# Kernel tuning notes

Hardware: AMD Instinct MI355X
Metric: run time of the kernel (lower is better)

The kernel has to match this reference:

```python
import jax, jax.numpy as jnp
import numpy as np

PIXEL_THRESHOLD = 0.4
FRACTION_THRESHOLD = 0.03
NUM_CLASSES = 20
N, H, W = 100, 640, 960
LOGIT_SCALE = 8.0  # makes the instance-axis softmax peaky enough to cross PIXEL_THRESHOLD


def setup_inputs() -> dict:
    key = jax.random.key(0)
    k1, k2, k3 = jax.random.split(key, 3)
    cls_prob = jax.random.uniform(k1, (N,), dtype=jnp.float32)
    mask_prob = jax.random.normal(k2, (N, H, W), dtype=jnp.float32) * LOGIT_SCALE
    cls_idx = jax.random.randint(k3, (N,), 0, NUM_CLASSES)
    return {"cls_prob": cls_prob, "mask_prob": mask_prob, "cls_idx": cls_idx}


def _mask_removal(cls_prob, mask_prob, cls_idx):
    # Sort instances by class confidence, descending (greedy NMS order).
    order = jnp.argsort(-cls_prob)
    cls_prob_s = cls_prob[order]          # [N]
    cls_idx_s = cls_idx[order]            # [N]
    raw_s = mask_prob[order]              # [N,H,W] pre-softmax logits (mask_prob_copy)
    # Per-pixel softmax over the instance axis (permutation-equivariant, so
    # softmax-then-sort == sort-then-softmax as in the original).
    sm = jax.nn.softmax(raw_s, axis=0)    # [N,H,W]

    def step(state, inp):
        panoptic, mask_image = state      # [H,W], [C,H,W]
        smi, rawi, ci = inp
        logit = (smi >= PIXEL_THRESHOLD).astype(rawi.dtype)   # binarized mask [H,W]
        mask_sum = logit.sum()
        curr = mask_image[ci]
        overlap = jnp.sum((curr >= 1.0) & (logit == 1.0)).astype(rawi.dtype) / jnp.maximum(mask_sum, 1.0)
        degenerate = (logit.max() == logit.min()) | (mask_sum == 0.0)
        skip = degenerate | (overlap > FRACTION_THRESHOLD)
        # assign only unclaimed panoptic pixels inside the binarized mask
        assign = (panoptic == 0.0) & (logit == 1.0) & jnp.logical_not(skip)
        keep_mask = jnp.where(assign, rawi, 0.0)              # use_mask_low_constant=False
        panoptic = jnp.where(assign, 1.0, panoptic)
        mask_image = mask_image.at[ci].add(jnp.where(assign, logit, 0.0))
        return (panoptic, mask_image), (keep_mask, jnp.logical_not(skip))

    init = (jnp.zeros((H, W), jnp.float32), jnp.zeros((NUM_CLASSES, H, W), jnp.float32))
    _, (keep_masks, keep_flags) = jax.lax.scan(step, init, (sm, raw_s, cls_idx_s))
    # Fixed-shape outputs: keep_flags marks which (sorted) instances survived;
    # dropped instances have all-zero keep_masks rows.
    return cls_prob_s, keep_masks, cls_idx_s, keep_flags


def reference(cls_prob, mask_prob, cls_idx):
    return _mask_removal(cls_prob, mask_prob, cls_idx)
```

## Files before the change

kernel.cpp:

```cpp
#include <hip/hip_runtime.h>
#include <cstdint>
#include <cstddef>

#define N_INST 100
#define HW (640 * 960)
#define PIX_THR 0.4f
#define FRAC_THR 0.03f
#define EPS_BORDER 5e-5f
#define FLAG_CAP 65536
#define L2E 1.4426950408889634f

#define CB 1200
#define ZB 680
#define GRID (CB + ZB)
#define CHUNK_F4 15360
#define CHUNK_ITER 120
#define NCHUNK 1000
#define FIN_BLOCKS 128

#define OUT_MASKS_OFF 100
#define OUT_CLSIDX_OFF (100 + (size_t)N_INST * HW)
#define OUT_FLAGS_OFF (100 + (size_t)N_INST * HW + N_INST)


__global__ __launch_bounds__(256) void k0_init(
    const float* __restrict__ cls_prob,
    const int* __restrict__ cls_idx,
    int* __restrict__ ord,
    int* __restrict__ rank_arr,
    float* __restrict__ out,
    unsigned* __restrict__ mask_sum,
    unsigned* __restrict__ ctrs,
    unsigned* __restrict__ pair_cnt) {
    int t = threadIdx.x;
    if (t < N_INST) {
        float pi = cls_prob[t];
        int rank = 0;
        for (int j = 0; j < N_INST; ++j) {
            float pj = cls_prob[j];
            rank += (pj > pi) || (pj == pi && j < t);
        }
        ord[rank] = t;
        rank_arr[t] = rank;
        out[rank] = pi;
        out[OUT_CLSIDX_OFF + rank] = (float)cls_idx[t];
        mask_sum[t] = 0u;
    }
    if (t < 3) ctrs[t] = 0u;
    for (int i = t; i < N_INST * N_INST; i += 256)
        pair_cnt[i] = 0u;
}

__global__ __launch_bounds__(128) void k1_fused(
    const float* __restrict__ mask,
    const int* __restrict__ rank_arr,
    unsigned* __restrict__ mask_sum,
    unsigned* __restrict__ pair_cnt,
    uint4* __restrict__ pvals,
    unsigned* __restrict__ flag_count,
    unsigned* __restrict__ flag_list,
    unsigned* __restrict__ zctr,
    float* __restrict__ out) {
    int t = threadIdx.x;
    __shared__ unsigned s_chunk;

    if (blockIdx.x < CB) {
        __shared__ int srank[N_INST];
        __shared__ unsigned ssum[N_INST];
        if (t < N_INST) {
            srank[t] = rank_arr[t];
            ssum[t] = 0u;
        }
        __syncthreads();

        int p0 = (blockIdx.x * 128 + t) * 4;
        const float* base = mask + p0;

        float S[4] = {0.0f, 0.0f, 0.0f, 0.0f};
        float m[4] = {-3.4e38f, -3.4e38f, -3.4e38f, -3.4e38f};
        float n[4] = {-3.4e38f, -3.4e38f, -3.4e38f, -3.4e38f};
        int ia[4] = {0, 0, 0, 0};
        int ib[4] = {0, 0, 0, 0};

#pragma unroll 10
        for (int i = 0; i < N_INST; ++i) {
            float4 v4 = *(const float4*)(base + (size_t)i * HW);
            float vv[4] = {v4.x, v4.y, v4.z, v4.w};
#pragma unroll
            for (int j = 0; j < 4; ++j) {
                float v = vv[j];
                S[j] += exp2f(v * L2E);
                bool gt = v > m[j];
                bool g2 = v > n[j];
                n[j] = fmaxf(n[j], fminf(m[j], v));
                ib[j] = gt ? ia[j] : (g2 ? i : ib[j]);
                ia[j] = gt ? i : ia[j];
                m[j] = fmaxf(m[j], v);
            }
        }

#pragma unroll
        for (int j = 0; j < 4; ++j) {
            int p = p0 + j;
            float e1 = exp2f(m[j] * L2E);
            float e2 = exp2f(n[j] * L2E);
            float t04 = 0.4f * S[j];
            float w = EPS_BORDER * S[j];
            bool q1 = e1 >= t04;
            bool border = (fabsf(e1 - t04) < w) || (q1 && fabsf(e2 - t04) < w);

            unsigned c = 0u;
            float vlo = 0.0f, vhi = 0.0f;
            if (border) {
                unsigned slot = atomicAdd(flag_count, 1u);
                if (slot < FLAG_CAP) flag_list[slot] = (unsigned)p;
            } else if (q1) {
                bool q2 = e2 >= t04;
                int r1 = srank[ia[j]];
                atomicAdd(&ssum[r1], 1u);
                if (q2) {
                    int r2 = srank[ib[j]];
                    atomicAdd(&ssum[r2], 1u);
                    int lo = min(r1, r2), hi = max(r1, r2);
                    atomicAdd(&pair_cnt[lo * N_INST + hi], 1u);
                    c = (unsigned)(lo + 1) | ((unsigned)(hi + 1) << 8);
                    vlo = (r1 < r2) ? m[j] : n[j];
                    vhi = (r1 < r2) ? n[j] : m[j];
                } else {
                    c = (unsigned)(r1 + 1);
                    vlo = m[j];
                }
            }
            pvals[p] = make_uint4(c, __float_as_uint(vlo), __float_as_uint(vhi), 0u);
        }

        __syncthreads();
        if (t < N_INST && ssum[t] != 0u)
            atomicAdd(&mask_sum[t], ssum[t]);
    }

    for (;;) {
        if (t == 0) s_chunk = atomicAdd(zctr, 1u);
        __syncthreads();
        unsigned c = s_chunk;
        __syncthreads();
        if (c >= NCHUNK) break;
        float4* dst = (float4*)(out + OUT_MASKS_OFF) + (size_t)c * CHUNK_F4 + t;
        const float4 z4 = make_float4(0.0f, 0.0f, 0.0f, 0.0f);
#pragma unroll 8
        for (int k = 0; k < CHUNK_ITER; ++k)
            dst[k * 128] = z4;
    }
}

__global__ __launch_bounds__(256) void k2_finish(
    const float* __restrict__ mask,
    const int* __restrict__ ord,
    const int* __restrict__ cls_idx,
    unsigned* __restrict__ mask_sum,
    unsigned* __restrict__ pair_cnt,
    uint4* __restrict__ pvals,
    const unsigned* __restrict__ flag_count,
    const unsigned* __restrict__ flag_list,
    unsigned* __restrict__ done,
    int* __restrict__ keep,
    float* __restrict__ out) {
    __shared__ int sord[N_INST];
    __shared__ unsigned s_last;
    int t = threadIdx.x;
    if (t < N_INST) sord[t] = ord[t];
    __syncthreads();

    unsigned nf = *flag_count;
    if (nf > FLAG_CAP) nf = FLAG_CAP;
    for (unsigned idx = blockIdx.x * 256 + t; idx < nf;
         idx += FIN_BLOCKS * 256) {
        int p = (int)flag_list[idx];
        float v[N_INST];
#pragma unroll
        for (int i = 0; i < N_INST; ++i)
            v[i] = mask[(size_t)sord[i] * HW + p];

        float m = v[0];
        int p1 = 0;
        float m2 = -3.4e38f;
        int p2 = 0;
#pragma unroll
        for (int i = 1; i < N_INST; ++i) {
            if (v[i] > m) { m2 = m; p2 = p1; m = v[i]; p1 = i; }
            else if (v[i] > m2) { m2 = v[i]; p2 = i; }
        }
        float d = 0.0f;
#pragma unroll
        for (int i = 0; i < N_INST; ++i)
            d += expf(v[i] - m);

        float sm1 = 1.0f / d;
        float sm2 = expf(m2 - m) / d;
        bool q1 = (sm1 >= PIX_THR);
        bool q2 = (sm2 >= PIX_THR);
        unsigned c = 0u;
        float vlo = 0.0f, vhi = 0.0f;
        if (q1) {
            atomicAdd(&mask_sum[p1], 1u);
            if (q2) {
                atomicAdd(&mask_sum[p2], 1u);
                int lo = min(p1, p2), hi = max(p1, p2);
                atomicAdd(&pair_cnt[lo * N_INST + hi], 1u);
                c = (unsigned)(lo + 1) | ((unsigned)(hi + 1) << 8);
                vlo = v[lo];
                vhi = v[hi];
            } else {
                c = (unsigned)(p1 + 1);
                vlo = v[p1];
            }
        }
        pvals[p] = make_uint4(c, __float_as_uint(vlo), __float_as_uint(vhi), 0u);
    }

    __threadfence();
    if (t == 0) s_last = atomicAdd(done, 1u);
    __syncthreads();
    if (s_last != FIN_BLOCKS - 1) return;
    __threadfence();

    __shared__ unsigned spair[N_INST * N_INST];
    __shared__ int scls[N_INST];
    __shared__ unsigned sms[N_INST];
    __shared__ int skeep[N_INST];
    for (int i = t; i < N_INST * N_INST; i += 256)
        spair[i] = pair_cnt[i];
    if (t < N_INST) {
        scls[t] = cls_idx[sord[t]];
        sms[t] = mask_sum[t];
    }
    __syncthreads();

    for (int b = 0; b < N_INST; ++b) {
        if (t < 64) {
            unsigned cnt = 0u;
            for (int a = t; a < b; a += 64)
                if (skeep[a] && scls[a] == scls[b])
                    cnt += spair[a * N_INST + b];
#pragma unroll
            for (int off = 32; off; off >>= 1)
                cnt += __shfl_down((int)cnt, off);
            if (t == 0) {
                unsigned ms = sms[b];
                float overlap = (float)cnt / fmaxf((float)ms, 1.0f);
                bool degen = (ms == 0u) || (ms == (unsigned)HW);
                bool skip = degen || (overlap > FRAC_THR);
                skeep[b] = skip ? 0 : 1;
            }
        }
        __syncthreads();
    }

    if (t < N_INST) {
        keep[t] = skeep[t];
        out[OUT_FLAGS_OFF + t] = (float)skeep[t];
    }
}

__global__ __launch_bounds__(256) void k3_scatter(
    const uint4* __restrict__ pvals,
    const int* __restrict__ keep,
    float* __restrict__ out) {
    __shared__ int skeep[N_INST];
    if (threadIdx.x < N_INST) skeep[threadIdx.x] = keep[threadIdx.x];
    __syncthreads();

    int p = blockIdx.x * 256 + threadIdx.x;
    uint4 pv = pvals[p];
    unsigned c = pv.x;
    if (c == 0u) return;
    int a = (int)(c & 0xFFu) - 1;
    int b = (int)(c >> 8) - 1;

    int inst;
    float val;
    if (skeep[a]) {
        inst = a;
        val = __uint_as_float(pv.y);
    } else if (b >= 0 && skeep[b]) {
        inst = b;
        val = __uint_as_float(pv.z);
    } else {
        return;
    }
    out[OUT_MASKS_OFF + (size_t)inst * HW + p] = val;
}

extern "C" void kernel_launch(void* const* d_in, const int* in_sizes, int n_in,
                              void* d_out, int out_size, void* d_ws, size_t ws_size,
                              hipStream_t stream) {
    const float* cls_prob = (const float*)d_in[0];
    const float* mask = (const float*)d_in[1];
    const int* cls_idx = (const int*)d_in[2];
    float* out = (float*)d_out;

    char* ws = (char*)d_ws;
    int* ord = (int*)(ws + 0);
    int* rank_arr = (int*)(ws + 512);
    int* keep = (int*)(ws + 1024);
    unsigned* mask_sum = (unsigned*)(ws + 1536);
    unsigned* ctrs = (unsigned*)(ws + 2048);
    unsigned* pair_cnt = (unsigned*)(ws + 4096);
    uint4* pvals = (uint4*)(ws + 65536);
    unsigned* flag_list = (unsigned*)(ws + 65536 + (size_t)HW * 16);

    unsigned* flag_count = &ctrs[0];
    unsigned* zctr = &ctrs[1];
    unsigned* done = &ctrs[2];

    k0_init<<<1, 256, 0, stream>>>(cls_prob, cls_idx, ord, rank_arr, out,
                                   mask_sum, ctrs, pair_cnt);
    k1_fused<<<GRID, 128, 0, stream>>>(mask, rank_arr, mask_sum, pair_cnt,
                                       pvals, flag_count, flag_list, zctr, out);
    k2_finish<<<FIN_BLOCKS, 256, 0, stream>>>(mask, ord, cls_idx, mask_sum,
                                              pair_cnt, pvals, flag_count,
                                              flag_list, done, keep, out);
    k3_scatter<<<HW / 256, 256, 0, stream>>>(pvals, keep, out);
}
```

Baseline: 259.6 us.

## Fold border-pixel fixup and greedy keep decision into the main kernel's last block

Merges the separate finish kernel into the main fused kernel: the last block to finish, found with a done counter, re-evaluates flagged border pixels and runs the sequential greedy keep/skip scan. This removes one kernel launch and its gap. The number of zeroing blocks also drops. In exchange, the border fixup now runs on a single 128-thread block instead of 128 blocks. It re-reads the 100 logits per pixel twice rather than caching them in registers, and the pair counts are read from global memory instead of shared memory, which could lengthen the serial tail.

```diff
diff --git a/kernel.cpp b/kernel.cpp
--- a/kernel.cpp
+++ b/kernel.cpp
@@ -11,12 +11,11 @@
 #define L2E 1.4426950408889634f
 
 #define CB 1200
-#define ZB 680
+#define ZB 480
 #define GRID (CB + ZB)
 #define CHUNK_F4 15360
 #define CHUNK_ITER 120
 #define NCHUNK 1000
-#define FIN_BLOCKS 128
 
 #define OUT_MASKS_OFF 100
 #define OUT_CLSIDX_OFF (100 + (size_t)N_INST * HW)
@@ -51,25 +50,32 @@
         pair_cnt[i] = 0u;
 }
 
-__global__ __launch_bounds__(128) void k1_fused(
+__global__ __launch_bounds__(128) void k1_mega(
     const float* __restrict__ mask,
     const int* __restrict__ rank_arr,
+    const int* __restrict__ ord,
+    const int* __restrict__ cls_idx,
     unsigned* __restrict__ mask_sum,
     unsigned* __restrict__ pair_cnt,
     uint4* __restrict__ pvals,
     unsigned* __restrict__ flag_count,
     unsigned* __restrict__ flag_list,
     unsigned* __restrict__ zctr,
+    unsigned* __restrict__ done,
+    int* __restrict__ keep,
     float* __restrict__ out) {
     int t = threadIdx.x;
     __shared__ unsigned s_chunk;
+    __shared__ unsigned s_last;
+    __shared__ int s_i[N_INST];
+    __shared__ unsigned s_u[N_INST];
+    __shared__ int scls[N_INST];
+    __shared__ int skp[N_INST];
 
     if (blockIdx.x < CB) {
-        __shared__ int srank[N_INST];
-        __shared__ unsigned ssum[N_INST];
         if (t < N_INST) {
-            srank[t] = rank_arr[t];
-            ssum[t] = 0u;
+            s_i[t] = rank_arr[t];
+            s_u[t] = 0u;
         }
         __syncthreads();
 
@@ -116,11 +122,11 @@
                 if (slot < FLAG_CAP) flag_list[slot] = (unsigned)p;
             } else if (q1) {
                 bool q2 = e2 >= t04;
-                int r1 = srank[ia[j]];
-                atomicAdd(&ssum[r1], 1u);
+                int r1 = s_i[ia[j]];
+                atomicAdd(&s_u[r1], 1u);
                 if (q2) {
-                    int r2 = srank[ib[j]];
-                    atomicAdd(&ssum[r2], 1u);
+                    int r2 = s_i[ib[j]];
+                    atomicAdd(&s_u[r2], 1u);
                     int lo = min(r1, r2), hi = max(r1, r2);
                     atomicAdd(&pair_cnt[lo * N_INST + hi], 1u);
                     c = (unsigned)(lo + 1) | ((unsigned)(hi + 1) << 8);
@@ -135,8 +141,8 @@
         }
 
         __syncthreads();
-        if (t < N_INST && ssum[t] != 0u)
-            atomicAdd(&mask_sum[t], ssum[t]);
+        if (t < N_INST && s_u[t] != 0u)
+            atomicAdd(&mask_sum[t], s_u[t]);
     }
 
     for (;;) {
@@ -151,50 +157,31 @@
         for (int k = 0; k < CHUNK_ITER; ++k)
             dst[k * 128] = z4;
     }
-}
-
-__global__ __launch_bounds__(256) void k2_finish(
-    const float* __restrict__ mask,
-    const int* __restrict__ ord,
-    const int* __restrict__ cls_idx,
-    unsigned* __restrict__ mask_sum,
-    unsigned* __restrict__ pair_cnt,
-    uint4* __restrict__ pvals,
-    const unsigned* __restrict__ flag_count,
-    const unsigned* __restrict__ flag_list,
-    unsigned* __restrict__ done,
-    int* __restrict__ keep,
-    float* __restrict__ out) {
-    __shared__ int sord[N_INST];
-    __shared__ unsigned s_last;
-    int t = threadIdx.x;
-    if (t < N_INST) sord[t] = ord[t];
-    __syncthreads();
-
+
+    __threadfence();
+    if (t == 0) s_last = atomicAdd(done, 1u);
+    __syncthreads();
+    if (s_last != GRID - 1) return;
+    __threadfence();
+
+    if (t < N_INST) s_i[t] = ord[t];
+    __syncthreads();
     unsigned nf = *flag_count;
     if (nf > FLAG_CAP) nf = FLAG_CAP;
-    for (unsigned idx = blockIdx.x * 256 + t; idx < nf;
-         idx += FIN_BLOCKS * 256) {
+    for (unsigned idx = t; idx < nf; idx += 128) {
         int p = (int)flag_list[idx];
-        float v[N_INST];
-#pragma unroll
-        for (int i = 0; i < N_INST; ++i)
-            v[i] = mask[(size_t)sord[i] * HW + p];
-
-        float m = v[0];
-        int p1 = 0;
-        float m2 = -3.4e38f;
-        int p2 = 0;
-#pragma unroll
-        for (int i = 1; i < N_INST; ++i) {
-            if (v[i] > m) { m2 = m; p2 = p1; m = v[i]; p1 = i; }
-            else if (v[i] > m2) { m2 = v[i]; p2 = i; }
+        float m = -3.4e38f, m2 = -3.4e38f;
+        int p1 = 0, p2 = 0;
+        for (int i = 0; i < N_INST; ++i) {
+            float v = mask[(size_t)s_i[i] * HW + p];
+            if (v > m) { m2 = m; p2 = p1; m = v; p1 = i; }
+            else if (v > m2) { m2 = v; p2 = i; }
         }
         float d = 0.0f;
-#pragma unroll
-        for (int i = 0; i < N_INST; ++i)
-            d += expf(v[i] - m);
-
+        for (int i = 0; i < N_INST; ++i) {
+            float v = mask[(size_t)s_i[i] * HW + p];
+            d += expf(v - m);
+        }
         float sm1 = 1.0f / d;
         float sm2 = expf(m2 - m) / d;
         bool q1 = (sm1 >= PIX_THR);
@@ -208,31 +195,21 @@
                 int lo = min(p1, p2), hi = max(p1, p2);
                 atomicAdd(&pair_cnt[lo * N_INST + hi], 1u);
                 c = (unsigned)(lo + 1) | ((unsigned)(hi + 1) << 8);
-                vlo = v[lo];
-                vhi = v[hi];
+                vlo = (lo == p1) ? m : m2;
+                vhi = (lo == p1) ? m2 : m;
             } else {
                 c = (unsigned)(p1 + 1);
-                vlo = v[p1];
+                vlo = m;
             }
         }
         pvals[p] = make_uint4(c, __float_as_uint(vlo), __float_as_uint(vhi), 0u);
     }
-
+    __syncthreads();
     __threadfence();
-    if (t == 0) s_last = atomicAdd(done, 1u);
-    __syncthreads();
-    if (s_last != FIN_BLOCKS - 1) return;
-    __threadfence();
-
-    __shared__ unsigned spair[N_INST * N_INST];
-    __shared__ int scls[N_INST];
-    __shared__ unsigned sms[N_INST];
-    __shared__ int skeep[N_INST];
-    for (int i = t; i < N_INST * N_INST; i += 256)
-        spair[i] = pair_cnt[i];
+
     if (t < N_INST) {
-        scls[t] = cls_idx[sord[t]];
-        sms[t] = mask_sum[t];
+        scls[t] = cls_idx[s_i[t]];
+        s_u[t] = mask_sum[t];
     }
     __syncthreads();
 
@@ -240,25 +217,25 @@
         if (t < 64) {
             unsigned cnt = 0u;
             for (int a = t; a < b; a += 64)
-                if (skeep[a] && scls[a] == scls[b])
-                    cnt += spair[a * N_INST + b];
+                if (skp[a] && scls[a] == scls[b])
+                    cnt += pair_cnt[a * N_INST + b];
 #pragma unroll
             for (int off = 32; off; off >>= 1)
                 cnt += __shfl_down((int)cnt, off);
             if (t == 0) {
-                unsigned ms = sms[b];
+                unsigned ms = s_u[b];
                 float overlap = (float)cnt / fmaxf((float)ms, 1.0f);
                 bool degen = (ms == 0u) || (ms == (unsigned)HW);
                 bool skip = degen || (overlap > FRAC_THR);
-                skeep[b] = skip ? 0 : 1;
+                skp[b] = skip ? 0 : 1;
             }
         }
         __syncthreads();
     }
 
     if (t < N_INST) {
-        keep[t] = skeep[t];
-        out[OUT_FLAGS_OFF + t] = (float)skeep[t];
+        keep[t] = skp[t];
+        out[OUT_FLAGS_OFF + t] = (float)skp[t];
     }
 }
 
@@ -315,10 +292,8 @@
 
     k0_init<<<1, 256, 0, stream>>>(cls_prob, cls_idx, ord, rank_arr, out,
                                    mask_sum, ctrs, pair_cnt);
-    k1_fused<<<GRID, 128, 0, stream>>>(mask, rank_arr, mask_sum, pair_cnt,
-                                       pvals, flag_count, flag_list, zctr, out);
-    k2_finish<<<FIN_BLOCKS, 256, 0, stream>>>(mask, ord, cls_idx, mask_sum,
-                                              pair_cnt, pvals, flag_count,
-                                              flag_list, done, keep, out);
+    k1_mega<<<GRID, 128, 0, stream>>>(mask, rank_arr, ord, cls_idx, mask_sum,
+                                      pair_cnt, pvals, flag_count, flag_list,
+                                      zctr, done, keep, out);
     k3_scatter<<<HW / 256, 256, 0, stream>>>(pvals, keep, out);
 }
```

After: 459.1 us. 1.77x slower.
